# Optimization experiments

Hardware: AMD Instinct MI355X
Metric: run time of the kernel (lower is better)

The kernel has to match this reference:

```python
import jax, jax.numpy as jnp
import numpy as np

D = 1e-6
B, N, E, K = 128, 512, 512, 256


def _lower_median_abs(x, axis):
    # torch.median returns the LOWER of the two middle values for even counts
    n = x.shape[axis]
    s = jnp.sort(jnp.abs(x), axis=axis)
    return jnp.take(s, (n - 1) // 2, axis=axis)


def _bounds_from_cauchy(head, errors, k):
    # errors: (B, E, *head.shape[1:]); E divisible by k in this config
    b, e = errors.shape[0], errors.shape[1]
    tail = errors.shape[2:]
    chunks = errors.reshape(b, e // k, k, *tail)
    l1 = _lower_median_abs(chunks, axis=2).sum(axis=1)
    return head - l1, head + l1


def _relaxed_exp(h, errs, noise, lb, ub):
    is_tight = ub == lb
    lam_s = (jnp.exp(ub) - jnp.exp(lb)) / (ub - lb + D)
    lam = jnp.minimum(lam_s, jnp.exp(lb + 1.0 - 0.1))
    ub0 = jnp.where(lam > lam_s, jnp.exp(lb) - lam * lb, jnp.exp(ub) - lam * ub)
    mu = 0.5 * (lam * (1.0 - jnp.log(lam)) + ub0)
    delta = 0.5 * (ub0 - lam * (1.0 - jnp.log(lam)))
    lam = jnp.where(is_tight, 0.0, lam)
    mu = jnp.where(is_tight, jnp.exp(ub), mu)
    delta = jnp.where(is_tight, 0.0, delta)
    new_head = h * lam + mu
    new_errs = jnp.concatenate([errs * lam[:, None], delta[:, None] * noise], axis=1)
    return new_head, new_errs


def _relaxed_log(h, errs, noise, lb, ub):
    is_tight = ub == lb
    lam_s = (jnp.log(ub) - jnp.log(lb + D)) / (ub - lb + D)
    lam = lam_s
    lb0 = jnp.where(lam < lam_s, jnp.log(ub) - ub * lam, jnp.log(lb + D) - lb * lam)
    mu = 0.5 * (-jnp.log(lam) - 1.0 + lb0)
    delta = 0.5 * (-jnp.log(lam) - 1.0 - lb0)
    lam = jnp.where(is_tight, 0.0, lam)
    mu = jnp.where(is_tight, jnp.log(ub), mu)
    delta = jnp.where(is_tight, 0.0, delta)
    new_head = h * lam + mu
    new_errs = jnp.concatenate([errs * lam[:, None], delta[:, None] * noise], axis=1)
    return new_head, new_errs


def setup_inputs() -> dict:
    key = jax.random.key(0)
    k1, k2, k3, k4 = jax.random.split(key, 4)
    curr_head = jax.random.normal(k1, (B, N), dtype=jnp.float32)
    # small error magnitudes keep exp/log relaxation bounds valid (lb of log stage > 0)
    curr_errors = 1e-3 * jax.random.normal(k2, (B * E, N), dtype=jnp.float32)
    cauchy_exp = jax.random.cauchy(k3, (B, K, N), dtype=jnp.float32)
    cauchy_log = jax.random.cauchy(k4, (B, K), dtype=jnp.float32)
    return {"curr_head": curr_head, "curr_errors": curr_errors,
            "cauchy_exp": cauchy_exp, "cauchy_log": cauchy_log, "k": K}


def reference(curr_head, curr_errors, cauchy_exp, cauchy_log, k):
    b, n = curr_head.shape
    max_head = jax.lax.stop_gradient(jnp.max(curr_head, axis=1, keepdims=True))  # (B,1)
    temp_head = curr_head - max_head                         # (B,N)
    errs = curr_errors.reshape(b, -1, n)                     # (B,E,N)
    lb, ub = _bounds_from_cauchy(temp_head, errs, k)
    exp_head, exp_errs = _relaxed_exp(temp_head, errs, cauchy_exp, lb, ub)  # (B,N),(B,E+K,N)
    exp_head = exp_head.sum(axis=1)                          # (B,)
    exp_errs = exp_errs.sum(axis=2)                          # (B,E+K)
    lb2, ub2 = _bounds_from_cauchy(exp_head, exp_errs, k)
    ls_head, ls_errs = _relaxed_log(exp_head, exp_errs, cauchy_log, lb2, ub2)  # (B,),(B,E+2K)
    ls_head = ls_head + max_head[:, 0]
    return ls_head, ls_errs.reshape(-1)
```

## Files before the change

### kernel.cpp

```cpp
#include <hip/hip_runtime.h>
#include <cstdint>
#include <cstddef>

#define BB 128
#define NN 512
#define EE 512
#define KK 256
#define STR 17

__device__ __forceinline__ float wave_reduce_max(float v) {
#pragma unroll
  for (int off = 32; off >= 1; off >>= 1) v = fmaxf(v, __shfl_xor(v, off, 64));
  return v;
}
__device__ __forceinline__ float wave_reduce_sum(float v) {
#pragma unroll
  for (int off = 32; off >= 1; off >>= 1) v += __shfl_xor(v, off, 64);
  return v;
}

template <int CTRL>
__device__ __forceinline__ float dppz(float x) {
  return __int_as_float(__builtin_amdgcn_update_dpp(0, __float_as_int(x), CTRL, 0xf, 0xf, false));
}
template <int CTRL>
__device__ __forceinline__ float dppi(float x) {
  return __int_as_float(__builtin_amdgcn_update_dpp(__float_as_int(x), __float_as_int(x), CTRL, 0xf, 0xf, false));
}
__device__ __forceinline__ float wave_sum64(float x) {
  x += dppz<0x111>(x); x += dppz<0x112>(x); x += dppz<0x114>(x); x += dppz<0x118>(x);
  x += dppz<0x142>(x); x += dppz<0x143>(x);
  return __int_as_float(__builtin_amdgcn_readlane(__float_as_int(x), 63));
}
__device__ __forceinline__ float wave_max64nn(float x) {
  x = fmaxf(x, dppz<0x111>(x)); x = fmaxf(x, dppz<0x112>(x));
  x = fmaxf(x, dppz<0x114>(x)); x = fmaxf(x, dppz<0x118>(x));
  x = fmaxf(x, dppz<0x142>(x)); x = fmaxf(x, dppz<0x143>(x));
  return __int_as_float(__builtin_amdgcn_readlane(__float_as_int(x), 63));
}
__device__ __forceinline__ float wave_min64(float x) {
  x = fminf(x, dppi<0x111>(x)); x = fminf(x, dppi<0x112>(x));
  x = fminf(x, dppi<0x114>(x)); x = fminf(x, dppi<0x118>(x));
  x = fminf(x, dppi<0x142>(x)); x = fminf(x, dppi<0x143>(x));
  return __int_as_float(__builtin_amdgcn_readlane(__float_as_int(x), 63));
}

__device__ __forceinline__ float wave_median256_fast(float a0, float a1, float a2, float a3) {
  float S = wave_sum64((a0 + a1) + (a2 + a3));
  float mean = S * 0.00390625f;
  float lo = 0.f, hi = S * 1.0000002f + 1e-37f;
  int c_lo = 0, c_hi = 256;
  float piv = 0.845f * mean;
  float ans = 0.f;
  bool have = false;
#pragma unroll 1
  for (int it = 0; it < 34; ++it) {
    if (!(piv > lo && piv < hi)) piv = 0.5f * (lo + hi);
    int cnt = __popcll(__ballot(a0 < piv)) + __popcll(__ballot(a1 < piv)) +
              __popcll(__ballot(a2 < piv)) + __popcll(__ballot(a3 < piv));
    if (cnt == 128) {
      float m = fmaxf(fmaxf(a0 < piv ? a0 : 0.f, a1 < piv ? a1 : 0.f),
                      fmaxf(a2 < piv ? a2 : 0.f, a3 < piv ? a3 : 0.f));
      ans = wave_max64nn(m); have = true; break;
    }
    if (cnt == 127) {
      float m = fminf(fminf(a0 >= piv ? a0 : 3.4e38f, a1 >= piv ? a1 : 3.4e38f),
                      fminf(a2 >= piv ? a2 : 3.4e38f, a3 >= piv ? a3 : 3.4e38f));
      ans = wave_min64(m); have = true; break;
    }
    if (cnt < 127) { lo = piv; c_lo = cnt; } else { hi = piv; c_hi = cnt; }
    if (it == 0) piv = piv + (127.5f - (float)cnt) * mean * 0.0077f;
    else piv = lo + (hi - lo) * ((127.5f - (float)c_lo) / (float)(c_hi - c_lo));
    if (it >= 10) piv = 0.5f * (lo + hi);
  }
  if (!have) {
    float m = fmaxf(fmaxf(a0 < hi ? a0 : 0.f, a1 < hi ? a1 : 0.f),
                    fmaxf(a2 < hi ? a2 : 0.f, a3 < hi ? a3 : 0.f));
    ans = wave_max64nn(m);
  }
  return ans;
}

__global__ __launch_bounds__(512, 8) void kfused(
    const float* __restrict__ head, const float* __restrict__ errs,
    float* __restrict__ ws_delta, float* __restrict__ ws_htpart,
    float* __restrict__ ws_epart) {
  __shared__ float tile[512 * STR];
  __shared__ float medbuf[32];
  __shared__ float lambuf[16];
  __shared__ float redm[8];
  const int blk = blockIdx.x;
  const int b = blk >> 5, g = blk & 31;
  const int n0 = g * 16;
  const int tid = threadIdx.x, wave = tid >> 6, lane = tid & 63;

  float m = head[(size_t)b * NN + tid];
  m = wave_reduce_max(m);
  if (lane == 0) redm[wave] = m;

  const int tr = tid >> 2, tc = (tid & 3) * 4;
  const float* src = errs + (size_t)b * EE * NN + n0 + tc;
#pragma unroll
  for (int i = 0; i < 4; ++i) {
    int row = i * 128 + tr;
    float4 v = *(const float4*)(src + (size_t)row * NN);
    float* dst = &tile[row * STR + tc];
    dst[0] = v.x; dst[1] = v.y; dst[2] = v.z; dst[3] = v.w;
  }
  __syncthreads();

#pragma unroll 1
  for (int j = 0; j < 4; ++j) {
    int p = wave * 4 + j;
    int col = p & 15;
    int rb = (p >> 4) * 256;
    float a0 = fabsf(tile[(rb + lane) * STR + col]);
    float a1 = fabsf(tile[(rb + lane + 64) * STR + col]);
    float a2 = fabsf(tile[(rb + lane + 128) * STR + col]);
    float a3 = fabsf(tile[(rb + lane + 192) * STR + col]);
    float med = wave_median256_fast(a0, a1, a2, a3);
    if (lane == 0) medbuf[p] = med;
  }
  __syncthreads();

  float htp = 0.f;
  if (tid < 16) {
    float hmax = fmaxf(fmaxf(fmaxf(redm[0], redm[1]), fmaxf(redm[2], redm[3])),
                       fmaxf(fmaxf(redm[4], redm[5]), fmaxf(redm[6], redm[7])));
    int n = n0 + tid;
    float l1 = medbuf[tid] + medbuf[16 + tid];
    float th = head[(size_t)b * NN + n] - hmax;
    float lb = th - l1, ub = th + l1;
    float lam, mu, delta;
    if (ub == lb) {
      lam = 0.f; mu = expf(ub); delta = 0.f;
    } else {
      float elb = expf(lb), eub = expf(ub);
      float lam_s = (eub - elb) / (ub - lb + 1e-6f);
      lam = fminf(lam_s, expf(lb + 0.9f));
      float ub0 = (lam > lam_s) ? (elb - lam * lb) : (eub - lam * ub);
      float t = lam * (1.f - logf(lam));
      mu = 0.5f * (t + ub0);
      delta = 0.5f * (ub0 - t);
    }
    lambuf[tid] = lam;
    ws_delta[(size_t)b * NN + n] = delta;
    htp = th * lam + mu;
  }
  if (wave == 0) {
    float s = wave_reduce_sum(htp);
    if (lane == 0) ws_htpart[b * 32 + g] = s;
  }
  __syncthreads();

  float s0 = 0.f;
#pragma unroll
  for (int j = 0; j < 16; ++j) s0 = fmaf(tile[tid * STR + j], lambuf[j], s0);
  ws_epart[((size_t)(b * 32 + g)) * 512 + tid] = s0;
}

__global__ __launch_bounds__(256) void kcexp(
    const float* __restrict__ cexp, const float* __restrict__ ws_delta,
    float* __restrict__ ws_ee2) {
  const int blk = blockIdx.x;
  const int b = blk >> 4, seg = blk & 15;
  const int wave = threadIdx.x >> 6, lane = threadIdx.x & 63;
  const float* wsrc = ws_delta + (size_t)b * NN;
  float4 wa = *(const float4*)(wsrc + 4 * lane);
  float4 wb = *(const float4*)(wsrc + 256 + 4 * lane);
  const int r0 = seg * 16 + wave * 4;
  const float* base = cexp + (size_t)b * KK * NN;
  float* out = ws_ee2 + (size_t)b * KK;
  float s0, s1, s2, s3;
  {
    const float* rp = base + (size_t)r0 * NN;
    float4 x = *(const float4*)(rp + 4 * lane);
    float4 y = *(const float4*)(rp + 256 + 4 * lane);
    s0 = x.x * wa.x + x.y * wa.y + x.z * wa.z + x.w * wa.w +
         y.x * wb.x + y.y * wb.y + y.z * wb.z + y.w * wb.w;
  }
  {
    const float* rp = base + (size_t)(r0 + 1) * NN;
    float4 x = *(const float4*)(rp + 4 * lane);
    float4 y = *(const float4*)(rp + 256 + 4 * lane);
    s1 = x.x * wa.x + x.y * wa.y + x.z * wa.z + x.w * wa.w +
         y.x * wb.x + y.y * wb.y + y.z * wb.z + y.w * wb.w;
  }
  {
    const float* rp = base + (size_t)(r0 + 2) * NN;
    float4 x = *(const float4*)(rp + 4 * lane);
    float4 y = *(const float4*)(rp + 256 + 4 * lane);
    s2 = x.x * wa.x + x.y * wa.y + x.z * wa.z + x.w * wa.w +
         y.x * wb.x + y.y * wb.y + y.z * wb.z + y.w * wb.w;
  }
  {
    const float* rp = base + (size_t)(r0 + 3) * NN;
    float4 x = *(const float4*)(rp + 4 * lane);
    float4 y = *(const float4*)(rp + 256 + 4 * lane);
    s3 = x.x * wa.x + x.y * wa.y + x.z * wa.z + x.w * wa.w +
         y.x * wb.x + y.y * wb.y + y.z * wb.z + y.w * wb.w;
  }
  s0 = wave_sum64(s0);
  s1 = wave_sum64(s1);
  s2 = wave_sum64(s2);
  s3 = wave_sum64(s3);
  if (lane == 0) {
    out[r0] = s0; out[r0 + 1] = s1; out[r0 + 2] = s2; out[r0 + 3] = s3;
  }
}

__global__ __launch_bounds__(256) void kreduce(
    const float* __restrict__ ws_epart, float* __restrict__ ws_ee1) {
  const int idx = blockIdx.x * 256 + threadIdx.x;
  const int b = idx >> 9, e = idx & 511;
  const float* pp = ws_epart + (size_t)b * 32 * 512 + e;
  float acc = 0.f;
#pragma unroll
  for (int g = 0; g < 32; ++g) acc += pp[g * 512];
  ws_ee1[idx] = acc;
}

__global__ __launch_bounds__(256) void kstage3(
    const float* __restrict__ head, const float* __restrict__ clog,
    const float* __restrict__ ws_htpart, const float* __restrict__ ws_ee1,
    const float* __restrict__ ws_ee2, float* __restrict__ out) {
  __shared__ float eb[768];
  __shared__ float redm[4];
  __shared__ float meds[3];
  __shared__ float sc[2];
  __shared__ float ehsh;
  const int b = blockIdx.x;
  const int tid = threadIdx.x, wave = tid >> 6, lane = tid & 63;

  float m = fmaxf(head[(size_t)b * NN + tid], head[(size_t)b * NN + 256 + tid]);
  m = wave_reduce_max(m);
  if (lane == 0) redm[wave] = m;

  eb[tid] = ws_ee1[(size_t)b * NN + tid];
  eb[tid + 256] = ws_ee1[(size_t)b * NN + 256 + tid];
  eb[tid + 512] = ws_ee2[(size_t)b * KK + tid];
  __syncthreads();

  if (wave < 3) {
    const float* p = eb + wave * 256;
    float a0 = fabsf(p[lane]), a1 = fabsf(p[lane + 64]);
    float a2 = fabsf(p[lane + 128]), a3 = fabsf(p[lane + 192]);
    float med = wave_median256_fast(a0, a1, a2, a3);
    if (lane == 0) meds[wave] = med;
  } else {
    float v = (lane < 32) ? ws_htpart[b * 32 + lane] : 0.f;
    v = wave_reduce_sum(v);
    if (lane == 0) ehsh = v;
  }
  __syncthreads();

  if (tid == 0) {
    float hmax = fmaxf(fmaxf(redm[0], redm[1]), fmaxf(redm[2], redm[3]));
    float eh = ehsh;
    float l1 = meds[0] + meds[1] + meds[2];
    float lb = eh - l1, ub = eh + l1;
    float lam, mu, delta;
    if (ub == lb) {
      lam = 0.f; mu = logf(ub); delta = 0.f;
    } else {
      float llb = logf(lb + 1e-6f);
      float lam_s = (logf(ub) - llb) / (ub - lb + 1e-6f);
      lam = lam_s;
      float lb0 = llb - lb * lam;
      float t = -logf(lam) - 1.f;
      mu = 0.5f * (t + lb0);
      delta = 0.5f * (t - lb0);
    }
    sc[0] = lam; sc[1] = delta;
    out[b] = eh * lam + mu + hmax;
  }
  __syncthreads();
  float lam = sc[0], delta = sc[1];
  float* ob = out + BB + (size_t)b * 1024;
  ob[tid] = eb[tid] * lam;
  ob[tid + 256] = eb[tid + 256] * lam;
  ob[tid + 512] = eb[tid + 512] * lam;
  ob[tid + 768] = delta * clog[(size_t)b * KK + tid];
}

extern "C" void kernel_launch(void* const* d_in, const int* in_sizes, int n_in,
                              void* d_out, int out_size, void* d_ws, size_t ws_size,
                              hipStream_t stream) {
  const float* head = (const float*)d_in[0];
  const float* errs = (const float*)d_in[1];
  const float* cexp = (const float*)d_in[2];
  const float* clog = (const float*)d_in[3];
  float* out = (float*)d_out;

  float* ws = (float*)d_ws;
  float* ws_delta = ws;
  float* ws_htpart = ws_delta + BB * NN;
  float* ws_ee2 = ws_htpart + BB * 32;
  float* ws_ee1 = ws_ee2 + BB * KK;
  float* ws_epart = ws_ee1 + BB * NN;

  hipLaunchKernelGGL(kfused, dim3(BB * 32), dim3(512), 0, stream,
                     head, errs, ws_delta, ws_htpart, ws_epart);
  hipLaunchKernelGGL(kcexp, dim3(BB * 16), dim3(256), 0, stream,
                     cexp, ws_delta, ws_ee2);
  hipLaunchKernelGGL(kreduce, dim3(256), dim3(256), 0, stream,
                     ws_epart, ws_ee1);
  hipLaunchKernelGGL(kstage3, dim3(BB), dim3(256), 0, stream,
                     head, clog, ws_htpart, ws_ee1, ws_ee2, out);
}
```

Measured before the change: 265.2 us.

## Double kfused block size and fold the partial-sum reduction into kstage3

Launches kfused with 1024 threads so each wave computes two column medians instead of four, and each thread loads half as many tile rows. This raises the number of resident waves per block to hide latency in the median search and global loads. It also removes the separate kreduce kernel: kstage3 now sums the 32 per-group partials itself, which saves a launch and an intermediate buffer. The cost is that this reduction runs across only 128 blocks, and the 1024-thread launch bound may tighten register allocation.

```diff
diff --git a/kernel.cpp b/kernel.cpp
--- a/kernel.cpp
+++ b/kernel.cpp
@@ -81,28 +81,28 @@
   return ans;
 }
 
-__global__ __launch_bounds__(512, 8) void kfused(
+__global__ __launch_bounds__(1024, 8) void kfused(
     const float* __restrict__ head, const float* __restrict__ errs,
     float* __restrict__ ws_delta, float* __restrict__ ws_htpart,
     float* __restrict__ ws_epart) {
   __shared__ float tile[512 * STR];
   __shared__ float medbuf[32];
   __shared__ float lambuf[16];
-  __shared__ float redm[8];
+  __shared__ float redm[16];
   const int blk = blockIdx.x;
   const int b = blk >> 5, g = blk & 31;
   const int n0 = g * 16;
   const int tid = threadIdx.x, wave = tid >> 6, lane = tid & 63;
 
-  float m = head[(size_t)b * NN + tid];
+  float m = (tid < NN) ? head[(size_t)b * NN + tid] : -3.4e38f;
   m = wave_reduce_max(m);
   if (lane == 0) redm[wave] = m;
 
   const int tr = tid >> 2, tc = (tid & 3) * 4;
   const float* src = errs + (size_t)b * EE * NN + n0 + tc;
 #pragma unroll
-  for (int i = 0; i < 4; ++i) {
-    int row = i * 128 + tr;
+  for (int i = 0; i < 2; ++i) {
+    int row = i * 256 + tr;
     float4 v = *(const float4*)(src + (size_t)row * NN);
     float* dst = &tile[row * STR + tc];
     dst[0] = v.x; dst[1] = v.y; dst[2] = v.z; dst[3] = v.w;
@@ -110,8 +110,8 @@
   __syncthreads();
 
 #pragma unroll 1
-  for (int j = 0; j < 4; ++j) {
-    int p = wave * 4 + j;
+  for (int j = 0; j < 2; ++j) {
+    int p = wave * 2 + j;
     int col = p & 15;
     int rb = (p >> 4) * 256;
     float a0 = fabsf(tile[(rb + lane) * STR + col]);
@@ -125,8 +125,11 @@
 
   float htp = 0.f;
   if (tid < 16) {
-    float hmax = fmaxf(fmaxf(fmaxf(redm[0], redm[1]), fmaxf(redm[2], redm[3])),
-                       fmaxf(fmaxf(redm[4], redm[5]), fmaxf(redm[6], redm[7])));
+    float hmax = fmaxf(
+        fmaxf(fmaxf(fmaxf(redm[0], redm[1]), fmaxf(redm[2], redm[3])),
+              fmaxf(fmaxf(redm[4], redm[5]), fmaxf(redm[6], redm[7]))),
+        fmaxf(fmaxf(fmaxf(redm[8], redm[9]), fmaxf(redm[10], redm[11])),
+              fmaxf(fmaxf(redm[12], redm[13]), fmaxf(redm[14], redm[15]))));
     int n = n0 + tid;
     float l1 = medbuf[tid] + medbuf[16 + tid];
     float th = head[(size_t)b * NN + n] - hmax;
@@ -153,10 +156,12 @@
   }
   __syncthreads();
 
-  float s0 = 0.f;
-#pragma unroll
-  for (int j = 0; j < 16; ++j) s0 = fmaf(tile[tid * STR + j], lambuf[j], s0);
-  ws_epart[((size_t)(b * 32 + g)) * 512 + tid] = s0;
+  if (tid < NN) {
+    float s0 = 0.f;
+#pragma unroll
+    for (int j = 0; j < 16; ++j) s0 = fmaf(tile[tid * STR + j], lambuf[j], s0);
+    ws_epart[((size_t)(b * 32 + g)) * 512 + tid] = s0;
+  }
 }
 
 __global__ __launch_bounds__(256) void kcexp(
@@ -209,20 +214,9 @@
   }
 }
 
-__global__ __launch_bounds__(256) void kreduce(
-    const float* __restrict__ ws_epart, float* __restrict__ ws_ee1) {
-  const int idx = blockIdx.x * 256 + threadIdx.x;
-  const int b = idx >> 9, e = idx & 511;
-  const float* pp = ws_epart + (size_t)b * 32 * 512 + e;
-  float acc = 0.f;
-#pragma unroll
-  for (int g = 0; g < 32; ++g) acc += pp[g * 512];
-  ws_ee1[idx] = acc;
-}
-
 __global__ __launch_bounds__(256) void kstage3(
     const float* __restrict__ head, const float* __restrict__ clog,
-    const float* __restrict__ ws_htpart, const float* __restrict__ ws_ee1,
+    const float* __restrict__ ws_htpart, const float* __restrict__ ws_epart,
     const float* __restrict__ ws_ee2, float* __restrict__ out) {
   __shared__ float eb[768];
   __shared__ float redm[4];
@@ -236,8 +230,15 @@
   m = wave_reduce_max(m);
   if (lane == 0) redm[wave] = m;
 
-  eb[tid] = ws_ee1[(size_t)b * NN + tid];
-  eb[tid + 256] = ws_ee1[(size_t)b * NN + 256 + tid];
+  float acc0 = 0.f, acc1 = 0.f;
+  const float* pp = ws_epart + (size_t)b * 32 * 512;
+#pragma unroll
+  for (int g = 0; g < 32; ++g) {
+    acc0 += pp[g * 512 + tid];
+    acc1 += pp[g * 512 + 256 + tid];
+  }
+  eb[tid] = acc0;
+  eb[tid + 256] = acc1;
   eb[tid + 512] = ws_ee2[(size_t)b * KK + tid];
   __syncthreads();
 
@@ -296,15 +297,12 @@
   float* ws_delta = ws;
   float* ws_htpart = ws_delta + BB * NN;
   float* ws_ee2 = ws_htpart + BB * 32;
-  float* ws_ee1 = ws_ee2 + BB * KK;
-  float* ws_epart = ws_ee1 + BB * NN;
-
-  hipLaunchKernelGGL(kfused, dim3(BB * 32), dim3(512), 0, stream,
+  float* ws_epart = ws_ee2 + BB * KK;
+
+  hipLaunchKernelGGL(kfused, dim3(BB * 32), dim3(1024), 0, stream,
                      head, errs, ws_delta, ws_htpart, ws_epart);
   hipLaunchKernelGGL(kcexp, dim3(BB * 16), dim3(256), 0, stream,
                      cexp, ws_delta, ws_ee2);
-  hipLaunchKernelGGL(kreduce, dim3(256), dim3(256), 0, stream,
-                     ws_epart, ws_ee1);
   hipLaunchKernelGGL(kstage3, dim3(BB), dim3(256), 0, stream,
-                     head, clog, ws_htpart, ws_ee1, ws_ee2, out);
-}
+                     head, clog, ws_htpart, ws_epart, ws_ee2, out);
+}
```

After: 275.5 us. 3.9% more time.
